# Kernel optimization log

Hardware: AMD Instinct MI355X
Metric: run time of the kernel (lower is better)

The kernel has to match this reference:

```python
import jax, jax.numpy as jnp
import numpy as np

NHEAD = 16
NUM_GROUPS = 4
EXPERTS_PER_GROUP = 2
LN_EPS = 1e-5


def _layernorm(x, g, b):
    mu = jnp.mean(x, axis=-1, keepdims=True)
    var = jnp.mean(jnp.square(x - mu), axis=-1, keepdims=True)
    return (x - mu) * jax.lax.rsqrt(var + LN_EPS) * g + b


def _mha(x, wi, bi, wo, bo):
    # torch nn.MultiheadAttention (batch_first): qkv = x @ in_proj_w.T + in_proj_b
    B, S, D = x.shape
    hd = D // NHEAD
    qkv = x @ wi.T + bi                      # [B,S,3D]
    q, k, v = jnp.split(qkv, 3, axis=-1)
    def heads(t):
        return t.reshape(B, S, NHEAD, hd).transpose(0, 2, 1, 3)  # [B,H,S,hd]
    q, k, v = heads(q), heads(k), heads(v)
    scores = jnp.einsum('bhqd,bhkd->bhqk', q, k) / jnp.sqrt(jnp.asarray(hd, x.dtype))
    attn = jax.nn.softmax(scores, axis=-1)
    o = jnp.einsum('bhqk,bhkd->bhqd', attn, v)
    o = o.transpose(0, 2, 1, 3).reshape(B, S, D)
    return o @ wo.T + bo


def _hier_moe(x, w_group, b_group, w_expert, b_expert, w1, b1, w2, b2):
    # Two-level top-1 routing: group gate -> expert gate within chosen group.
    B, S, D = x.shape
    xt = x.reshape(B * S, D)                 # [T,D]
    T = xt.shape[0]
    E = NUM_GROUPS * EXPERTS_PER_GROUP

    gp = jax.nn.softmax(xt @ w_group + b_group, axis=-1)          # [T,G]
    g_idx = jnp.argmax(gp, axis=-1)                                # [T]
    g_prob = jnp.max(gp, axis=-1)                                  # [T]

    elog = jnp.einsum('td,gde->tge', xt, w_expert) + b_expert      # [T,G,Epg]
    ep = jax.nn.softmax(elog, axis=-1)
    ep_sel = jnp.take_along_axis(ep, g_idx[:, None, None], axis=1)[:, 0, :]  # [T,Epg]
    e_idx_local = jnp.argmax(ep_sel, axis=-1)                      # [T]
    e_prob = jnp.max(ep_sel, axis=-1)                              # [T]

    flat_e = g_idx * EXPERTS_PER_GROUP + e_idx_local               # [T]
    combine = jax.nn.one_hot(flat_e, E, dtype=xt.dtype) * (g_prob * e_prob)[:, None]  # [T,E]

    # Dense dispatch (reference): run every expert on all tokens, combine with one-hot weights.
    h = jax.nn.relu(jnp.einsum('td,edf->etf', xt, w1) + b1[:, None, :])   # [E,T,Fff]
    y = jnp.einsum('etf,efd->etd', h, w2) + b2[:, None, :]                # [E,T,D]
    out = jnp.einsum('te,etd->td', combine, y)                            # [T,D]
    return out.reshape(B, S, D)


def setup_inputs() -> dict:
    key = jax.random.key(0)
    ks = jax.random.split(key, 8)
    B, S, D, F = 2, 1024, 1024, 2048
    G, Epg = NUM_GROUPS, EXPERTS_PER_GROUP
    E = G * Epg
    sc = lambda fan: 1.0 / np.sqrt(fan)
    return {
        'x': jax.random.normal(ks[0], (B, S, D), jnp.float32),
        'in_proj_w': jax.random.normal(ks[1], (3 * D, D), jnp.float32) * sc(D),
        'in_proj_b': jnp.zeros((3 * D,), jnp.float32),
        'out_proj_w': jax.random.normal(ks[2], (D, D), jnp.float32) * sc(D),
        'out_proj_b': jnp.zeros((D,), jnp.float32),
        'ln1_g': jnp.ones((D,), jnp.float32),
        'ln1_b': jnp.zeros((D,), jnp.float32),
        'ln2_g': jnp.ones((D,), jnp.float32),
        'ln2_b': jnp.zeros((D,), jnp.float32),
        'w_group': jax.random.normal(ks[3], (D, G), jnp.float32) * sc(D),
        'b_group': jnp.zeros((G,), jnp.float32),
        'w_expert': jax.random.normal(ks[4], (G, D, Epg), jnp.float32) * sc(D),
        'b_expert': jnp.zeros((G, Epg), jnp.float32),
        'w1': jax.random.normal(ks[5], (E, D, F), jnp.float32) * sc(D),
        'b1': jnp.zeros((E, F), jnp.float32),
        'w2': jax.random.normal(ks[6], (E, F, D), jnp.float32) * sc(F),
        'b2': jnp.zeros((E, D), jnp.float32),
    }


def reference(x, in_proj_w, in_proj_b, out_proj_w, out_proj_b,
              ln1_g, ln1_b, ln2_g, ln2_b,
              w_group, b_group, w_expert, b_expert, w1, b1, w2, b2):
    # Dropout p=0.1 is identity in eval mode.
    attn_out = _mha(x, in_proj_w, in_proj_b, out_proj_w, out_proj_b)
    x = _layernorm(x + attn_out, ln1_g, ln1_b)
    moe_out = _hier_moe(x, w_group, b_group, w_expert, b_expert, w1, b1, w2, b2)
    x = _layernorm(x + moe_out, ln2_g, ln2_b)
    return x
```

## Files before the change

kernel.cpp:

```cpp
#include <hip/hip_runtime.h>
#include <hip/hip_bf16.h>

#define TT 2048
#define DD 1024
#define FF 2048
#define SS 1024
#define NHD 16
#define HDD 64
#define NG 4
#define EPG 2
#define NE 8

#define QSC 0.18033688011112042f

typedef __attribute__((ext_vector_type(8))) short bf16x8;
typedef __attribute__((ext_vector_type(4))) float f32x4;
typedef __attribute__((ext_vector_type(4))) unsigned short ush4;

__device__ __forceinline__ unsigned short f2bf(float x) {
    unsigned int u = __float_as_uint(x);
    u = (u + 0x7fffu + ((u >> 16) & 1u)) >> 16;
    return (unsigned short)u;
}
__device__ __forceinline__ float bf2f(unsigned short h) {
    return __uint_as_float((unsigned int)h << 16);
}

__device__ __forceinline__ float wave_sum(float s) {
#pragma unroll
    for (int off = 32; off > 0; off >>= 1) s += __shfl_xor(s, off);
    return s;
}

__device__ __forceinline__ void gl16(const void* g, void* l) {
    auto gp = reinterpret_cast<const unsigned int __attribute__((address_space(1)))*>(
        (unsigned long long)g);
    auto lp = reinterpret_cast<unsigned int __attribute__((address_space(3)))*>(
        (unsigned int)(unsigned long long)l);
    __builtin_amdgcn_global_load_lds(gp, lp, 16, 0, 0);
}

__global__ __launch_bounds__(256) void split_bf16_kernel(
    const float* __restrict__ in, unsigned short* __restrict__ hi,
    unsigned short* __restrict__ lo, int n4)
{
    const int i = blockIdx.x * 256 + threadIdx.x;
    if (i >= n4) return;
    const float4 v = ((const float4*)in)[i];
    float vv[4] = {v.x, v.y, v.z, v.w};
    ush4 h, l;
#pragma unroll
    for (int j = 0; j < 4; ++j) {
        const unsigned short hb = f2bf(vv[j]);
        ((unsigned short*)&h)[j] = hb;
        ((unsigned short*)&l)[j] = f2bf(vv[j] - bf2f(hb));
    }
    ((ush4*)hi)[i] = h;
    ((ush4*)lo)[i] = l;
}

__global__ __launch_bounds__(256, 3) void gemm_split_kernel(
    const unsigned short* __restrict__ Ah, const unsigned short* __restrict__ Al,
    const unsigned short* __restrict__ Bh, const unsigned short* __restrict__ Bl,
    const float* __restrict__ bias, const float* __restrict__ resid,
    float* __restrict__ C, unsigned short* __restrict__ Chi,
    unsigned short* __restrict__ Clo, int qscale_n, int M, int N, int K)
{
    __shared__ unsigned short sAh[128 * 64];
    __shared__ unsigned short sAl[128 * 64];
    __shared__ unsigned short sBh[64 * 64];
    __shared__ unsigned short sBl[64 * 64];
    const int tid = threadIdx.x;
    const int lane = tid & 63, wid = tid >> 6;
    const int l15 = lane & 15, lg = lane >> 4;
    const int n0 = blockIdx.x << 6, m0 = blockIdx.y << 7;
    const int kper = K / gridDim.z;
    const int kbeg = blockIdx.z * kper, kend = kbeg + kper;
    float* __restrict__ Cz = C ? (C + (size_t)blockIdx.z * M * N) : C;

    f32x4 acc[2][4];
#pragma unroll
    for (int mi = 0; mi < 2; ++mi)
#pragma unroll
        for (int ni = 0; ni < 4; ++ni) acc[mi][ni] = (f32x4){0.f, 0.f, 0.f, 0.f};

    for (int k0 = kbeg; k0 < kend; k0 += 64) {
#pragma unroll
        for (int r = 0; r < 4; ++r) {
            const int s = (r << 8) + tid;
            const int row = s >> 3;
            const int cs = (s & 7) ^ (row & 7);
            const int lb = (s & ~63) << 3;
            const size_t ga = (size_t)(m0 + row) * K + k0 + (cs << 3);
            gl16(Ah + ga, &sAh[lb]);
            gl16(Al + ga, &sAl[lb]);
        }
#pragma unroll
        for (int r = 0; r < 2; ++r) {
            const int s = (r << 8) + tid;
            const int row = s >> 3;
            const int cs = (s & 7) ^ (row & 7);
            const int lb = (s & ~63) << 3;
            const size_t gb = (size_t)(n0 + row) * K + k0 + (cs << 3);
            gl16(Bh + gb, &sBh[lb]);
            gl16(Bl + gb, &sBl[lb]);
        }
        __syncthreads();
#pragma unroll
        for (int ks = 0; ks < 2; ++ks) {
            bf16x8 ah[2], al[2], bh[4], bl[4];
            const int ac = (ks << 2) + lg;
#pragma unroll
            for (int i = 0; i < 2; ++i) {
                const int ar = (wid << 5) + (i << 4) + l15;
                const int pa = ((ar << 3) | (ac ^ (ar & 7))) << 3;
                ah[i] = *(const bf16x8*)&sAh[pa];
                al[i] = *(const bf16x8*)&sAl[pa];
            }
#pragma unroll
            for (int i = 0; i < 4; ++i) {
                const int br = (i << 4) + l15;
                const int pb = ((br << 3) | (ac ^ (br & 7))) << 3;
                bh[i] = *(const bf16x8*)&sBh[pb];
                bl[i] = *(const bf16x8*)&sBl[pb];
            }
#pragma unroll
            for (int mi = 0; mi < 2; ++mi)
#pragma unroll
                for (int ni = 0; ni < 4; ++ni) {
                    acc[mi][ni] = __builtin_amdgcn_mfma_f32_16x16x32_bf16(ah[mi], bh[ni], acc[mi][ni], 0, 0, 0);
                    acc[mi][ni] = __builtin_amdgcn_mfma_f32_16x16x32_bf16(ah[mi], bl[ni], acc[mi][ni], 0, 0, 0);
                    acc[mi][ni] = __builtin_amdgcn_mfma_f32_16x16x32_bf16(al[mi], bh[ni], acc[mi][ni], 0, 0, 0);
                }
        }
        __syncthreads();
    }
#pragma unroll
    for (int mi = 0; mi < 2; ++mi)
#pragma unroll
        for (int ni = 0; ni < 4; ++ni)
#pragma unroll
            for (int r2 = 0; r2 < 4; ++r2) {
                const int m = m0 + (wid << 5) + (mi << 4) + (lg << 2) + r2;
                const int n = n0 + (ni << 4) + l15;
                float v = acc[mi][ni][r2];
                if (bias) v += bias[n];
                if (resid) v += resid[(size_t)m * N + n];
                const size_t idx = (size_t)m * N + n;
                if (Chi) {
                    if (n < qscale_n) v *= QSC;
                    const unsigned short hb = f2bf(v);
                    Chi[idx] = hb;
                    Clo[idx] = f2bf(v - bf2f(hb));
                } else {
                    Cz[idx] = v;
                }
            }
}

__global__ __launch_bounds__(256) void vtrans_kernel(
    const unsigned short* __restrict__ srch, const unsigned short* __restrict__ srcl,
    unsigned short* __restrict__ dsth, unsigned short* __restrict__ dstl)
{
    __shared__ unsigned short tile[64][65];
    const unsigned short* __restrict__ src = blockIdx.z ? srcl : srch;
    unsigned short* __restrict__ dst = blockIdx.z ? dstl : dsth;
    const int bh = blockIdx.y, b = bh >> 4, h = bh & 15;
    const int s0 = blockIdx.x << 6;
    const int tid = threadIdx.x;
#pragma unroll
    for (int r = 0; r < 2; ++r) {
        const int sl = tid + (r << 8);
        const int rr = sl >> 3, c8 = (sl & 7) << 3;
        const bf16x8 v = *(const bf16x8*)(src + (size_t)(b * SS + s0 + rr) * 3072 + 2048 + h * HDD + c8);
#pragma unroll
        for (int j = 0; j < 8; ++j) tile[rr][c8 + j] = ((const unsigned short*)&v)[j];
    }
    __syncthreads();
#pragma unroll
    for (int r = 0; r < 2; ++r) {
        const int sl = tid + (r << 8);
        const int d = sl >> 3, s8 = (sl & 7) << 3;
        bf16x8 o;
#pragma unroll
        for (int j = 0; j < 8; ++j) ((unsigned short*)&o)[j] = tile[s8 + j][d];
        *(bf16x8*)(dst + (size_t)(bh * HDD + d) * SS + s0 + s8) = o;
    }
}

__global__ __launch_bounds__(256, 4) void attn_mfma_kernel(
    const unsigned short* __restrict__ qh, const unsigned short* __restrict__ ql,
    const unsigned short* __restrict__ vth, const unsigned short* __restrict__ vtl,
    float* __restrict__ opart, float* __restrict__ mpart, float* __restrict__ lpart)
{
    __shared__ unsigned short sKh[4096], sKl[4096];
    __shared__ unsigned short sVh[4096], sVl[4096];
    const int bh = blockIdx.y, b = bh >> 4, h = bh & 15;
    const int q0 = blockIdx.x << 6;
    const int z = blockIdx.z;
    const int tid = threadIdx.x, lane = tid & 63, w = tid >> 6;
    const int l15 = lane & 15, lg = lane >> 4;

#pragma unroll
    for (int r = 0; r < 2; ++r) {
        const int s = (r << 8) + tid;
        const int row = s >> 3;
        const int cs = (s & 7) ^ (row & 7);
        const int lb = (s & ~63) << 3;
        const size_t gq = (size_t)(b * SS + q0 + row) * 3072 + h * HDD + (cs << 3);
        gl16(qh + gq, &sKh[lb]);
        gl16(ql + gq, &sKl[lb]);
    }
    __syncthreads();
    bf16x8 qah[2], qal[2];
#pragma unroll
    for (int ks = 0; ks < 2; ++ks) {
        const int ar = (w << 4) + l15;
        const int ac = (ks << 2) + lg;
        const int pa = ((ar << 3) | (ac ^ (ar & 7))) << 3;
        qah[ks] = *(const bf16x8*)&sKh[pa];
        qal[ks] = *(const bf16x8*)&sKl[pa];
    }
    __syncthreads();

    f32x4 accO[4];
#pragma unroll
    for (int nt = 0; nt < 4; ++nt) accO[nt] = (f32x4){0.f, 0.f, 0.f, 0.f};
    float m_run = -3.0e38f, l_run = 0.f;

    const int kvbeg = z << 9;
    for (int kv0 = kvbeg; kv0 < kvbeg + 512; kv0 += 64) {
#pragma unroll
        for (int r = 0; r < 2; ++r) {
            const int s = (r << 8) + tid;
            const int row = s >> 3;
            const int cs = (s & 7) ^ (row & 7);
            const int lb = (s & ~63) << 3;
            const size_t gk = (size_t)(b * SS + kv0 + row) * 3072 + DD + h * HDD + (cs << 3);
            gl16(qh + gk, &sKh[lb]);
            gl16(ql + gk, &sKl[lb]);
            const size_t gv = (size_t)(bh * HDD + row) * SS + kv0 + (cs << 3);
            gl16(vth + gv, &sVh[lb]);
            gl16(vtl + gv, &sVl[lb]);
        }
        __syncthreads();

        f32x4 sacc[4];
#pragma unroll
        for (int i = 0; i < 4; ++i) sacc[i] = (f32x4){0.f, 0.f, 0.f, 0.f};
        __builtin_amdgcn_s_setprio(1);
#pragma unroll
        for (int ks = 0; ks < 2; ++ks) {
            const int ac = (ks << 2) + lg;
#pragma unroll
            for (int i = 0; i < 4; ++i) {
                const int br = (i << 4) + l15;
                const int pb = ((br << 3) | (ac ^ (br & 7))) << 3;
                const bf16x8 kbh = *(const bf16x8*)&sKh[pb];
                const bf16x8 kbl = *(const bf16x8*)&sKl[pb];
                sacc[i] = __builtin_amdgcn_mfma_f32_16x16x32_bf16(kbh, qah[ks], sacc[i], 0, 0, 0);
                sacc[i] = __builtin_amdgcn_mfma_f32_16x16x32_bf16(kbh, qal[ks], sacc[i], 0, 0, 0);
                sacc[i] = __builtin_amdgcn_mfma_f32_16x16x32_bf16(kbl, qah[ks], sacc[i], 0, 0, 0);
            }
        }
        __builtin_amdgcn_s_setprio(0);
        __syncthreads();

        float mx = sacc[0][0];
#pragma unroll
        for (int i = 0; i < 4; ++i)
#pragma unroll
            for (int r2 = 0; r2 < 4; ++r2) mx = fmaxf(mx, sacc[i][r2]);
        mx = fmaxf(mx, __shfl_xor(mx, 16));
        mx = fmaxf(mx, __shfl_xor(mx, 32));
        const bool skip = __all(mx <= m_run + 8.0f);
        float mn, corr;
        if (skip) {
            mn = m_run; corr = 1.0f;
        } else {
            mn = fmaxf(m_run, mx);
            corr = exp2f(m_run - mn);
            m_run = mn;
        }
        float ls = 0.f;
        const int qrow = (w << 4) | l15;
#pragma unroll
        for (int i = 0; i < 4; ++i) {
            ush4 hp, lp;
#pragma unroll
            for (int r2 = 0; r2 < 4; ++r2) {
                const float p = exp2f(sacc[i][r2] - mn);
                ls += p;
                const unsigned short hb = (unsigned short)(__float_as_uint(p) >> 16);
                hp[r2] = hb;
                lp[r2] = (unsigned short)(__float_as_uint(p - bf2f(hb)) >> 16);
            }
            const int kvb = (i << 4) + (lg << 2);
            const int idx = (qrow << 6) + (((kvb >> 3) ^ (qrow & 7)) << 3) + (kvb & 7);
            *(ush4*)&sKh[idx] = hp;
            *(ush4*)&sKl[idx] = lp;
        }
        ls += __shfl_xor(ls, 16);
        ls += __shfl_xor(ls, 32);
        if (skip) {
            l_run += ls;
        } else {
            l_run = l_run * corr + ls;
            float c4[4];
#pragma unroll
            for (int r2 = 0; r2 < 4; ++r2)
                c4[r2] = __shfl(corr, (lane & 48) | ((lg << 2) + r2));
#pragma unroll
            for (int nt = 0; nt < 4; ++nt)
#pragma unroll
                for (int r2 = 0; r2 < 4; ++r2) accO[nt][r2] *= c4[r2];
        }

        __builtin_amdgcn_s_setprio(1);
#pragma unroll
        for (int ks = 0; ks < 2; ++ks) {
            const int qq = (w << 4) + l15;
            const int slot = (ks << 2) + lg;
            const int pidx = (qq << 6) + ((slot ^ (qq & 7)) << 3);
            const bf16x8 pah = *(const bf16x8*)&sKh[pidx];
            const bf16x8 pal = *(const bf16x8*)&sKl[pidx];
            const int ac = (ks << 2) + lg;
#pragma unroll
            for (int nt = 0; nt < 4; ++nt) {
                const int dr = (nt << 4) + l15;
                const int pv = ((dr << 3) | (ac ^ (dr & 7))) << 3;
                const bf16x8 vbh = *(const bf16x8*)&sVh[pv];
                const bf16x8 vbl = *(const bf16x8*)&sVl[pv];
                accO[nt] = __builtin_amdgcn_mfma_f32_16x16x32_bf16(pah, vbh, accO[nt], 0, 0, 0);
                accO[nt] = __builtin_amdgcn_mfma_f32_16x16x32_bf16(pah, vbl, accO[nt], 0, 0, 0);
                accO[nt] = __builtin_amdgcn_mfma_f32_16x16x32_bf16(pal, vbh, accO[nt], 0, 0, 0);
            }
        }
        __builtin_amdgcn_s_setprio(0);
        __syncthreads();
    }

#pragma unroll
    for (int nt = 0; nt < 4; ++nt)
#pragma unroll
        for (int r2 = 0; r2 < 4; ++r2) {
            const int qq = q0 + (w << 4) + (lg << 2) + r2;
            const int dd = h * HDD + (nt << 4) + l15;
            opart[((size_t)z * TT + b * SS + qq) * DD + dd] = accO[nt][r2];
        }
    if (lane < 16) {
        const int qq = q0 + (w << 4) + lane;
        const int idx = z * (32 * SS) + bh * SS + qq;
        mpart[idx] = m_run;
        lpart[idx] = l_run;
    }
}

__global__ __launch_bounds__(256) void attn_combine_kernel(
    const float* __restrict__ opart, const float* __restrict__ mpart,
    const float* __restrict__ lpart, unsigned short* __restrict__ ohi,
    unsigned short* __restrict__ olo)
{
    const int t = blockIdx.x;
    const int tid = threadIdx.x;
    const int b = t >> 10, q = t & 1023;
    const int d0 = tid << 2;
    const int bh = (b << 4) + (d0 >> 6);
    const int mi = bh * SS + q;
    const float m0 = mpart[mi], m1 = mpart[32 * SS + mi];
    const float l0 = lpart[mi], l1 = lpart[32 * SS + mi];
    const float m = fmaxf(m0, m1);
    const float e0 = exp2f(m0 - m), e1 = exp2f(m1 - m);
    const float inv = 1.0f / (l0 * e0 + l1 * e1);
    const float4 a = *(const float4*)(opart + (size_t)t * DD + d0);
    const float4 c = *(const float4*)(opart + (size_t)(TT + t) * DD + d0);
    const float vv[4] = { (a.x * e0 + c.x * e1) * inv, (a.y * e0 + c.y * e1) * inv,
                          (a.z * e0 + c.z * e1) * inv, (a.w * e0 + c.w * e1) * inv };
    ush4 hh, ll;
#pragma unroll
    for (int j = 0; j < 4; ++j) {
        const unsigned short hb = f2bf(vv[j]);
        hh[j] = hb;
        ll[j] = f2bf(vv[j] - bf2f(hb));
    }
    *(ush4*)(ohi + (size_t)t * DD + d0) = hh;
    *(ush4*)(olo + (size_t)t * DD + d0) = ll;
}

__global__ __launch_bounds__(256) void ln_kernel(
    const float* __restrict__ in, const float* __restrict__ gamma,
    const float* __restrict__ beta, float* __restrict__ outf)
{
    const int t = blockIdx.x;
    const int tid = threadIdx.x;
    __shared__ float red[8];
    const float4 v = ((const float4*)(in + (size_t)t * DD))[tid];
    float s = v.x + v.y + v.z + v.w;
    s = wave_sum(s);
    const int wid = tid >> 6, lane = tid & 63;
    if (lane == 0) red[wid] = s;
    __syncthreads();
    const float mu = (red[0] + red[1] + red[2] + red[3]) * (1.0f / DD);
    const float d0 = v.x - mu, d1 = v.y - mu, d2 = v.z - mu, d3 = v.w - mu;
    float q = d0 * d0 + d1 * d1 + d2 * d2 + d3 * d3;
    q = wave_sum(q);
    if (lane == 0) red[4 + wid] = q;
    __syncthreads();
    const float var = (red[4] + red[5] + red[6] + red[7]) * (1.0f / DD);
    const float rstd = 1.0f / sqrtf(var + 1e-5f);
    const float4 g4 = ((const float4*)gamma)[tid];
    const float4 b4 = ((const float4*)beta)[tid];
    float4 ov = { d0 * rstd * g4.x + b4.x, d1 * rstd * g4.y + b4.y,
                  d2 * rstd * g4.z + b4.z, d3 * rstd * g4.w + b4.w };
    ((float4*)(outf + (size_t)t * DD))[tid] = ov;
}

__global__ __launch_bounds__(256) void ln_route_kernel(
    const float* __restrict__ x, const float* __restrict__ p0,
    const float* __restrict__ p1, const float* __restrict__ bo,
    const float* __restrict__ gamma, const float* __restrict__ beta,
    float* __restrict__ outf, unsigned short* __restrict__ outb,
    const float* __restrict__ wg, const float* __restrict__ bg,
    const float* __restrict__ we, const float* __restrict__ be,
    int* __restrict__ eid, float* __restrict__ gate, int* __restrict__ counts)
{
    const int t = blockIdx.x;
    const int tid = threadIdx.x;
    __shared__ float red[8];
    __shared__ float red2[4][12];
    const float4 xv = ((const float4*)(x + (size_t)t * DD))[tid];
    const float4 a4 = ((const float4*)(p0 + (size_t)t * DD))[tid];
    const float4 c4v = ((const float4*)(p1 + (size_t)t * DD))[tid];
    const float4 bo4 = ((const float4*)bo)[tid];
    const float4 v = { xv.x + a4.x + c4v.x + bo4.x, xv.y + a4.y + c4v.y + bo4.y,
                       xv.z + a4.z + c4v.z + bo4.z, xv.w + a4.w + c4v.w + bo4.w };
    float s = v.x + v.y + v.z + v.w;
    s = wave_sum(s);
    const int wid = tid >> 6, lane = tid & 63;
    if (lane == 0) red[wid] = s;
    __syncthreads();
    const float mu = (red[0] + red[1] + red[2] + red[3]) * (1.0f / DD);
    const float d0 = v.x - mu, d1 = v.y - mu, d2 = v.z - mu, d3 = v.w - mu;
    float q = d0 * d0 + d1 * d1 + d2 * d2 + d3 * d3;
    q = wave_sum(q);
    if (lane == 0) red[4 + wid] = q;
    __syncthreads();
    const float var = (red[4] + red[5] + red[6] + red[7]) * (1.0f / DD);
    const float rstd = 1.0f / sqrtf(var + 1e-5f);
    const float4 g4 = ((const float4*)gamma)[tid];
    const float4 b4 = ((const float4*)beta)[tid];
    const float o0 = d0 * rstd * g4.x + b4.x;
    const float o1 = d1 * rstd * g4.y + b4.y;
    const float o2 = d2 * rstd * g4.z + b4.z;
    const float o3 = d3 * rstd * g4.w + b4.w;
    float4 ov = {o0, o1, o2, o3};
    ((float4*)(outf + (size_t)t * DD))[tid] = ov;
    ush4 wv = { f2bf(o0), f2bf(o1), f2bf(o2), f2bf(o3) };
    *(ush4*)(outb + (size_t)t * DD + (tid << 2)) = wv;

    float pz[12];
#pragma unroll
    for (int k = 0; k < 12; ++k) pz[k] = 0.f;
    const float xo[4] = {o0, o1, o2, o3};
#pragma unroll
    for (int j = 0; j < 4; ++j) {
        const int c = (tid << 2) + j;
        const float xvv = xo[j];
        const float4 wgv = *(const float4*)(wg + c * NG);
        pz[0] = fmaf(xvv, wgv.x, pz[0]);
        pz[1] = fmaf(xvv, wgv.y, pz[1]);
        pz[2] = fmaf(xvv, wgv.z, pz[2]);
        pz[3] = fmaf(xvv, wgv.w, pz[3]);
#pragma unroll
        for (int g = 0; g < NG; ++g) {
            const float2 wev = *(const float2*)(we + ((size_t)g * DD + c) * EPG);
            pz[4 + 2 * g]     = fmaf(xvv, wev.x, pz[4 + 2 * g]);
            pz[4 + 2 * g + 1] = fmaf(xvv, wev.y, pz[4 + 2 * g + 1]);
        }
    }
#pragma unroll
    for (int k = 0; k < 12; ++k) pz[k] = wave_sum(pz[k]);
    if (lane == 0) {
#pragma unroll
        for (int k = 0; k < 12; ++k) red2[wid][k] = pz[k];
    }
    __syncthreads();
    if (tid == 0) {
        float zs[12];
#pragma unroll
        for (int k = 0; k < 12; ++k)
            zs[k] = red2[0][k] + red2[1][k] + red2[2][k] + red2[3][k];
        float z[NG];
#pragma unroll
        for (int g = 0; g < NG; ++g) z[g] = zs[g] + bg[g];
        int gi = 0; float zb = z[0];
#pragma unroll
        for (int g = 1; g < NG; ++g) if (z[g] > zb) { zb = z[g]; gi = g; }
        float se = 0.f;
#pragma unroll
        for (int g = 0; g < NG; ++g) se += __expf(z[g] - zb);
        const float gprob = 1.0f / se;
        float e0 = 0.f, e1 = 0.f;
#pragma unroll
        for (int g = 0; g < NG; ++g) {
            if (g == gi) {
                e0 = zs[4 + 2 * g] + be[g * EPG + 0];
                e1 = zs[4 + 2 * g + 1] + be[g * EPG + 1];
            }
        }
        const int ei = (e1 > e0) ? 1 : 0;
        const float ehi = ei ? e1 : e0, elo = ei ? e0 : e1;
        const float eprob = 1.0f / (1.0f + __expf(elo - ehi));
        eid[t] = gi * EPG + ei;
        gate[t] = gprob * eprob;
        atomicAdd(&counts[gi * EPG + ei], 1);
    }
}

__global__ void zero_counts_kernel(int* __restrict__ counts) {
    if (threadIdx.x < NE) counts[threadIdx.x] = 0;
}

__global__ __launch_bounds__(256) void route_scatter_kernel(
    const int* __restrict__ eid, const int* __restrict__ counts,
    int* __restrict__ offs, int* __restrict__ perm)
{
    __shared__ int loff[NE + 1];
    __shared__ int lcur[NE];
    if (threadIdx.x == 0) {
        int run = 0;
        for (int e = 0; e < NE; ++e) { loff[e] = run; lcur[e] = run; run += counts[e]; }
        loff[NE] = run;
    }
    __syncthreads();
    for (int t = threadIdx.x; t < TT; t += 256) {
        const int slot = atomicAdd(&lcur[eid[t]], 1);
        perm[slot] = t;
    }
    if (threadIdx.x <= NE) offs[threadIdx.x] = loff[threadIdx.x];
}

__global__ __launch_bounds__(256) void transpose_bf16_kernel(
    const float* __restrict__ in, unsigned short* __restrict__ out, int R, int C)
{
    __shared__ unsigned short tile[64][72];
    const int c0 = blockIdx.x << 6, r0 = blockIdx.y << 6;
    const size_t bo = (size_t)blockIdx.z * R * C;
    const int tid = threadIdx.x;
#pragma unroll
    for (int p = 0; p < 4; ++p) {
        const int s = (p << 8) + tid;
        const int rr = s >> 4, cc = (s & 15) << 2;
        const float4 v = *(const float4*)(in + bo + (size_t)(r0 + rr) * C + c0 + cc);
        tile[rr][cc + 0] = f2bf(v.x);
        tile[rr][cc + 1] = f2bf(v.y);
        tile[rr][cc + 2] = f2bf(v.z);
        tile[rr][cc + 3] = f2bf(v.w);
    }
    __syncthreads();
#pragma unroll
    for (int p = 0; p < 2; ++p) {
        const int s = (p << 8) + tid;
        const int cc = s >> 3, rr = (s & 7) << 3;
        bf16x8 o;
#pragma unroll
        for (int j = 0; j < 8; ++j) ((unsigned short*)&o)[j] = tile[rr + j][cc];
        *(bf16x8*)(out + bo + (size_t)(c0 + cc) * R + r0 + rr) = o;
    }
}

__global__ __launch_bounds__(256, 3) void moe_gemm1_kernel(
    const unsigned short* __restrict__ x1b, const unsigned short* __restrict__ w1t,
    const float* __restrict__ b1, const int* __restrict__ offs,
    const int* __restrict__ perm, unsigned short* __restrict__ hbuf)
{
    const int e = blockIdx.y >> 4, mt = blockIdx.y & 15;
    const int row0 = offs[e] + (mt << 7);
    const int rend = offs[e + 1];
    if (row0 >= rend) return;
    const int valid = min(rend - row0, 128);
    const int n0 = blockIdx.x << 6;
    __shared__ unsigned short sA[2][128 * 64];
    __shared__ unsigned short sB[2][64 * 64];
    const int tid = threadIdx.x;
    const int lane = tid & 63, wid = tid >> 6;
    const int l15 = lane & 15, lg = lane >> 4;
    const int wr = wid >> 1, wc = wid & 1;

    size_t abase[4];
    int albs[4];
#pragma unroll
    for (int r = 0; r < 4; ++r) {
        const int s = (r << 8) + tid;
        const int row = s >> 3;
        const int cs = (s & 7) ^ (row & 7);
        albs[r] = (s & ~63) << 3;
        const int tk = perm[min(row0 + row, rend - 1)];
        abase[r] = (size_t)tk * DD + (cs << 3);
    }
    size_t bbase[2];
    int blbs[2];
#pragma unroll
    for (int r = 0; r < 2; ++r) {
        const int s = (r << 8) + tid;
        const int row = s >> 3;
        const int cs = (s & 7) ^ (row & 7);
        blbs[r] = (s & ~63) << 3;
        bbase[r] = ((size_t)e * FF + n0 + row) * DD + (cs << 3);
    }

    f32x4 acc[4][2];
#pragma unroll
    for (int mi = 0; mi < 4; ++mi)
#pragma unroll
        for (int ni = 0; ni < 2; ++ni) acc[mi][ni] = (f32x4){0.f, 0.f, 0.f, 0.f};

#pragma unroll
    for (int r = 0; r < 4; ++r) gl16(x1b + abase[r], &sA[0][albs[r]]);
#pragma unroll
    for (int r = 0; r < 2; ++r) gl16(w1t + bbase[r], &sB[0][blbs[r]]);
    __syncthreads();
    int cur = 0;
    for (int k0 = 0; k0 < DD; k0 += 64) {
        const int nxt = k0 + 64;
        if (nxt < DD) {
#pragma unroll
            for (int r = 0; r < 4; ++r) gl16(x1b + abase[r] + nxt, &sA[cur ^ 1][albs[r]]);
#pragma unroll
            for (int r = 0; r < 2; ++r) gl16(w1t + bbase[r] + nxt, &sB[cur ^ 1][blbs[r]]);
        }
#pragma unroll
        for (int ks = 0; ks < 2; ++ks) {
            const int ac = (ks << 2) + lg;
            bf16x8 a[4], bb[2];
#pragma unroll
            for (int mi = 0; mi < 4; ++mi) {
                const int ar = (wr << 6) + (mi << 4) + l15;
                const int pa = ((ar << 3) | (ac ^ (ar & 7))) << 3;
                a[mi] = *(const bf16x8*)&sA[cur][pa];
            }
#pragma unroll
            for (int ni = 0; ni < 2; ++ni) {
                const int br = (wc << 5) + (ni << 4) + l15;
                const int pb = ((br << 3) | (ac ^ (br & 7))) << 3;
                bb[ni] = *(const bf16x8*)&sB[cur][pb];
            }
#pragma unroll
            for (int mi = 0; mi < 4; ++mi)
#pragma unroll
                for (int ni = 0; ni < 2; ++ni)
                    acc[mi][ni] = __builtin_amdgcn_mfma_f32_16x16x32_bf16(a[mi], bb[ni], acc[mi][ni], 0, 0, 0);
        }
        __syncthreads();
        cur ^= 1;
    }

    const float* bias = b1 + e * FF + n0;
#pragma unroll
    for (int mi = 0; mi < 4; ++mi)
#pragma unroll
        for (int ni = 0; ni < 2; ++ni) {
            const int n = (wc << 5) + (ni << 4) + l15;
#pragma unroll
            for (int r2 = 0; r2 < 4; ++r2) {
                const int m = (wr << 6) + (mi << 4) + (lg << 2) + r2;
                if (m < valid) {
                    float v = fmaxf(acc[mi][ni][r2] + bias[n], 0.f);
                    hbuf[(size_t)(row0 + m) * FF + n0 + n] = f2bf(v);
                }
            }
        }
}

__global__ __launch_bounds__(256, 3) void moe_gemm2_kernel(
    const unsigned short* __restrict__ hbuf, const unsigned short* __restrict__ w2t,
    const int* __restrict__ offs, float* __restrict__ p0, float* __restrict__ p1)
{
    const int e = blockIdx.y >> 4, mt = blockIdx.y & 15;
    const int row0 = offs[e] + (mt << 7);
    const int rend = offs[e + 1];
    if (row0 >= rend) return;
    const int valid = min(rend - row0, 128);
    const int n0 = blockIdx.x << 6;
    const int z = blockIdx.z;
    float* __restrict__ pbuf = z ? p1 : p0;
    __shared__ unsigned short sA[2][128 * 64];
    __shared__ unsigned short sB[2][64 * 64];
    const int tid = threadIdx.x;
    const int lane = tid & 63, wid = tid >> 6;
    const int l15 = lane & 15, lg = lane >> 4;
    const int wr = wid >> 1, wc = wid & 1;

    size_t abase[4];
    int albs[4];
#pragma unroll
    for (int r = 0; r < 4; ++r) {
        const int s = (r << 8) + tid;
        const int row = s >> 3;
        const int cs = (s & 7) ^ (row & 7);
        albs[r] = (s & ~63) << 3;
        abase[r] = (size_t)min(row0 + row, rend - 1) * FF + (cs << 3);
    }
    size_t bbase[2];
    int blbs[2];
#pragma unroll
    for (int r = 0; r < 2; ++r) {
        const int s = (r << 8) + tid;
        const int row = s >> 3;
        const int cs = (s & 7) ^ (row & 7);
        blbs[r] = (s & ~63) << 3;
        bbase[r] = ((size_t)e * DD + n0 + row) * FF + (cs << 3);
    }

    f32x4 acc[4][2];
#pragma unroll
    for (int mi = 0; mi < 4; ++mi)
#pragma unroll
        for (int ni = 0; ni < 2; ++ni) acc[mi][ni] = (f32x4){0.f, 0.f, 0.f, 0.f};

    const int kbeg = z << 10, kend = kbeg + 1024;
#pragma unroll
    for (int r = 0; r < 4; ++r) gl16(hbuf + abase[r] + kbeg, &sA[0][albs[r]]);
#pragma unroll
    for (int r = 0; r < 2; ++r) gl16(w2t + bbase[r] + kbeg, &sB[0][blbs[r]]);
    __syncthreads();
    int cur = 0;
    for (int k0 = kbeg; k0 < kend; k0 += 64) {
        const int nxt = k0 + 64;
        if (nxt < kend) {
#pragma unroll
            for (int r = 0; r < 4; ++r) gl16(hbuf + abase[r] + nxt, &sA[cur ^ 1][albs[r]]);
#pragma unroll
            for (int r = 0; r < 2; ++r) gl16(w2t + bbase[r] + nxt, &sB[cur ^ 1][blbs[r]]);
        }
#pragma unroll
        for (int ks = 0; ks < 2; ++ks) {
            const int ac = (ks << 2) + lg;
            bf16x8 a[4], bb[2];
#pragma unroll
            for (int mi = 0; mi < 4; ++mi) {
                const int ar = (wr << 6) + (mi << 4) + l15;
                const int pa = ((ar << 3) | (ac ^ (ar & 7))) << 3;
                a[mi] = *(const bf16x8*)&sA[cur][pa];
            }
#pragma unroll
            for (int ni = 0; ni < 2; ++ni) {
                const int br = (wc << 5) + (ni << 4) + l15;
                const int pb = ((br << 3) | (ac ^ (br & 7))) << 3;
                bb[ni] = *(const bf16x8*)&sB[cur][pb];
            }
#pragma unroll
            for (int mi = 0; mi < 4; ++mi)
#pragma unroll
                for (int ni = 0; ni < 2; ++ni)
                    acc[mi][ni] = __builtin_amdgcn_mfma_f32_16x16x32_bf16(a[mi], bb[ni], acc[mi][ni], 0, 0, 0);
        }
        __syncthreads();
        cur ^= 1;
    }

#pragma unroll
    for (int mi = 0; mi < 4; ++mi)
#pragma unroll
        for (int ni = 0; ni < 2; ++ni) {
            const int n = (wc << 5) + (ni << 4) + l15;
#pragma unroll
            for (int r2 = 0; r2 < 4; ++r2) {
                const int m = (wr << 6) + (mi << 4) + (lg << 2) + r2;
                if (m < valid) pbuf[(size_t)(row0 + m) * DD + n0 + n] = acc[mi][ni][r2];
            }
        }
}

__global__ __launch_bounds__(256) void moe2_combine_kernel(
    const float* __restrict__ p0, const float* __restrict__ p1,
    const int* __restrict__ offs, const int* __restrict__ perm,
    const float* __restrict__ gate, const float* __restrict__ b2,
    const float* __restrict__ x1, float* __restrict__ res2)
{
    const int s = blockIdx.x;
    const int tid = threadIdx.x;
    int e = 0;
#pragma unroll
    for (int g = 1; g < NE; ++g) e += (s >= offs[g]) ? 1 : 0;
    const int tk = perm[s];
    const float gt = gate[tk];
    const int c0 = tid << 2;
    const float4 a  = *(const float4*)(p0 + (size_t)s * DD + c0);
    const float4 b  = *(const float4*)(p1 + (size_t)s * DD + c0);
    const float4 bb = *(const float4*)(b2 + (size_t)e * DD + c0);
    const float4 xx = *(const float4*)(x1 + (size_t)tk * DD + c0);
    float4 o = { xx.x + gt * (a.x + b.x + bb.x), xx.y + gt * (a.y + b.y + bb.y),
                 xx.z + gt * (a.z + b.z + bb.z), xx.w + gt * (a.w + b.w + bb.w) };
    *(float4*)(res2 + (size_t)tk * DD + c0) = o;
}

extern "C" void kernel_launch(void* const* d_in, const int* in_sizes, int n_in,
                              void* d_out, int out_size, void* d_ws, size_t ws_size,
                              hipStream_t stream)
{
    (void)in_sizes; (void)n_in; (void)out_size; (void)ws_size;
    const float* x   = (const float*)d_in[0];
    const float* wi  = (const float*)d_in[1];
    const float* bi  = (const float*)d_in[2];
    const float* wo  = (const float*)d_in[3];
    const float* bo  = (const float*)d_in[4];
    const float* g1  = (const float*)d_in[5];
    const float* be1 = (const float*)d_in[6];
    const float* g2  = (const float*)d_in[7];
    const float* be2 = (const float*)d_in[8];
    const float* wgr = (const float*)d_in[9];
    const float* bgr = (const float*)d_in[10];
    const float* wex = (const float*)d_in[11];
    const float* bex = (const float*)d_in[12];
    const float* w1  = (const float*)d_in[13];
    const float* b1  = (const float*)d_in[14];
    const float* w2  = (const float*)d_in[15];
    const float* b2  = (const float*)d_in[16];
    float* out = (float*)d_out;

    char* ws = (char*)d_ws;
    unsigned short* qkvh  = (unsigned short*)(ws + 0);
    unsigned short* qkvl  = (unsigned short*)(ws + 12582912);
    unsigned short* hbuf  = (unsigned short*)(ws + 0);
    float* res2           = (float*)(ws + 8388608);
    unsigned short* vth   = (unsigned short*)(ws + 25165824);
    unsigned short* vtl   = (unsigned short*)(ws + 29360128);
    float* x1             = (float*)(ws + 41943040);
    unsigned short* x1b   = (unsigned short*)(ws + 50331648);
    unsigned short* w1t   = (unsigned short*)(ws + 54525952);
    unsigned short* w2t   = (unsigned short*)(ws + 88080384);
    char* misc = ws + 121634816;
    int*   eid    = (int*)(misc);
    float* gate   = (float*)(misc + 8192);
    int*   perm   = (int*)(misc + 16384);
    int*   counts = (int*)(misc + 24576);
    int*   offs   = (int*)(misc + 24640);

    unsigned short* xs_hi = (unsigned short*)(ws + 33554432);
    unsigned short* xs_lo = (unsigned short*)(ws + 33554432 + 4194304);
    unsigned short* wi_hi = (unsigned short*)(ws + 54525952);
    unsigned short* wi_lo = (unsigned short*)(ws + 54525952 + 6291456);
    unsigned short* o_hi  = (unsigned short*)(ws + 41943040);
    unsigned short* o_lo  = (unsigned short*)(ws + 41943040 + 4194304);
    unsigned short* wo_hi = (unsigned short*)(ws + 88080384);
    unsigned short* wo_lo = (unsigned short*)(ws + 88080384 + 2097152);

    float* opart = (float*)(ws + 54525952);
    float* mpart = (float*)(ws + 54525952 + 16777216);
    float* lpart = (float*)(ws + 54525952 + 17039360);

    float* oproj = (float*)(ws + 0);

    float* mp0 = (float*)(ws + 16777216);
    float* mp1 = (float*)(ws + 25165824);

    zero_counts_kernel<<<dim3(1), dim3(64), 0, stream>>>(counts);

    split_bf16_kernel<<<dim3((TT * DD / 4 + 255) / 256), dim3(256), 0, stream>>>(x, xs_hi, xs_lo, TT * DD / 4);
    split_bf16_kernel<<<dim3((3 * DD * DD / 4 + 255) / 256), dim3(256), 0, stream>>>(wi, wi_hi, wi_lo, 3 * DD * DD / 4);
    gemm_split_kernel<<<dim3(3 * DD / 64, TT / 128, 1), dim3(256), 0, stream>>>(
        xs_hi, xs_lo, wi_hi, wi_lo, bi, (const float*)nullptr,
        (float*)nullptr, qkvh, qkvl, DD, TT, 3 * DD, DD);

    vtrans_kernel<<<dim3(SS / 64, 2 * NHD, 2), dim3(256), 0, stream>>>(qkvh, qkvl, vth, vtl);

    attn_mfma_kernel<<<dim3(SS / 64, 2 * NHD, 2), dim3(256), 0, stream>>>(
        qkvh, qkvl, vth, vtl, opart, mpart, lpart);
    attn_combine_kernel<<<dim3(TT), dim3(256), 0, stream>>>(opart, mpart, lpart, o_hi, o_lo);

    split_bf16_kernel<<<dim3((DD * DD / 4 + 255) / 256), dim3(256), 0, stream>>>(wo, wo_hi, wo_lo, DD * DD / 4);
    gemm_split_kernel<<<dim3(DD / 64, TT / 128, 2), dim3(256), 0, stream>>>(
        o_hi, o_lo, wo_hi, wo_lo, (const float*)nullptr, (const float*)nullptr,
        oproj, (unsigned short*)nullptr, (unsigned short*)nullptr, 0, TT, DD, DD);

    ln_route_kernel<<<dim3(TT), dim3(256), 0, stream>>>(
        x, oproj, oproj + (size_t)TT * DD, bo, g1, be1, x1, x1b,
        wgr, bgr, wex, bex, eid, gate, counts);
    route_scatter_kernel<<<dim3(1), dim3(256), 0, stream>>>(eid, counts, offs, perm);

    transpose_bf16_kernel<<<dim3(FF / 64, DD / 64, NE), dim3(256), 0, stream>>>(w1, w1t, DD, FF);
    transpose_bf16_kernel<<<dim3(DD / 64, FF / 64, NE), dim3(256), 0, stream>>>(w2, w2t, FF, DD);

    moe_gemm1_kernel<<<dim3(FF / 64, NE * 16), dim3(256), 0, stream>>>(x1b, w1t, b1, offs, perm, hbuf);
    moe_gemm2_kernel<<<dim3(DD / 64, NE * 16, 2), dim3(256), 0, stream>>>(hbuf, w2t, offs, mp0, mp1);
    moe2_combine_kernel<<<dim3(TT), dim3(256), 0, stream>>>(mp0, mp1, offs, perm, gate, b2, x1, res2);

    ln_kernel<<<dim3(TT), dim3(256), 0, stream>>>(res2, g2, be2, out);
}
```

Before: 253.0 us.

## Double attention query tile per block and merge small prep kernels

The attention kernel now processes 128 query rows per block, two 16-row groups per wave, so each K/V tile loaded into LDS is reused twice. P gets its own LDS buffers and occupancy drops to 2 blocks per CU. Separately, the three bf16 split launches plus the counts-zeroing kernel are merged into one launch, and the two weight transposes into one. This cuts launch overhead and K/V reload traffic at the cost of more registers and LDS per block and half as many attention blocks.

Result: faster. 241.6 us (-4.5%).

```diff
diff --git a/kernel.cpp b/kernel.cpp
--- a/kernel.cpp
+++ b/kernel.cpp
@@ -40,23 +40,36 @@
     __builtin_amdgcn_global_load_lds(gp, lp, 16, 0, 0);
 }
 
-__global__ __launch_bounds__(256) void split_bf16_kernel(
-    const float* __restrict__ in, unsigned short* __restrict__ hi,
-    unsigned short* __restrict__ lo, int n4)
-{
+#define NX4 (TT * DD / 4)
+#define NWI4 (3 * DD * DD / 4)
+#define NWO4 (DD * DD / 4)
+__global__ __launch_bounds__(256) void split3_kernel(
+    const float* __restrict__ x, const float* __restrict__ wi,
+    const float* __restrict__ wo,
+    unsigned short* __restrict__ xs_hi, unsigned short* __restrict__ xs_lo,
+    unsigned short* __restrict__ wi_hi, unsigned short* __restrict__ wi_lo,
+    unsigned short* __restrict__ wo_hi, unsigned short* __restrict__ wo_lo,
+    int* __restrict__ counts)
+{
+    if (blockIdx.x == 0 && threadIdx.x < NE) counts[threadIdx.x] = 0;
     const int i = blockIdx.x * 256 + threadIdx.x;
-    if (i >= n4) return;
-    const float4 v = ((const float4*)in)[i];
+    const float* in;
+    unsigned short *hi, *lo;
+    int j;
+    if (i < NX4) { in = x; hi = xs_hi; lo = xs_lo; j = i; }
+    else if (i < NX4 + NWI4) { in = wi; hi = wi_hi; lo = wi_lo; j = i - NX4; }
+    else { in = wo; hi = wo_hi; lo = wo_lo; j = i - NX4 - NWI4; }
+    const float4 v = ((const float4*)in)[j];
     float vv[4] = {v.x, v.y, v.z, v.w};
     ush4 h, l;
 #pragma unroll
-    for (int j = 0; j < 4; ++j) {
-        const unsigned short hb = f2bf(vv[j]);
-        ((unsigned short*)&h)[j] = hb;
-        ((unsigned short*)&l)[j] = f2bf(vv[j] - bf2f(hb));
-    }
-    ((ush4*)hi)[i] = h;
-    ((ush4*)lo)[i] = l;
+    for (int k = 0; k < 4; ++k) {
+        const unsigned short hb = f2bf(vv[k]);
+        ((unsigned short*)&h)[k] = hb;
+        ((unsigned short*)&l)[k] = f2bf(vv[k] - bf2f(hb));
+    }
+    ((ush4*)hi)[j] = h;
+    ((ush4*)lo)[j] = l;
 }
 
 __global__ __launch_bounds__(256, 3) void gemm_split_kernel(
@@ -188,45 +201,49 @@
     }
 }
 
-__global__ __launch_bounds__(256, 4) void attn_mfma_kernel(
+__global__ __launch_bounds__(256, 2) void attn_mfma_kernel(
     const unsigned short* __restrict__ qh, const unsigned short* __restrict__ ql,
     const unsigned short* __restrict__ vth, const unsigned short* __restrict__ vtl,
     float* __restrict__ opart, float* __restrict__ mpart, float* __restrict__ lpart)
 {
     __shared__ unsigned short sKh[4096], sKl[4096];
     __shared__ unsigned short sVh[4096], sVl[4096];
+    __shared__ unsigned short sPh[8192], sPl[8192];
     const int bh = blockIdx.y, b = bh >> 4, h = bh & 15;
-    const int q0 = blockIdx.x << 6;
+    const int q0 = blockIdx.x << 7;
     const int z = blockIdx.z;
     const int tid = threadIdx.x, lane = tid & 63, w = tid >> 6;
     const int l15 = lane & 15, lg = lane >> 4;
 
 #pragma unroll
-    for (int r = 0; r < 2; ++r) {
+    for (int r = 0; r < 4; ++r) {
         const int s = (r << 8) + tid;
         const int row = s >> 3;
         const int cs = (s & 7) ^ (row & 7);
         const int lb = (s & ~63) << 3;
         const size_t gq = (size_t)(b * SS + q0 + row) * 3072 + h * HDD + (cs << 3);
-        gl16(qh + gq, &sKh[lb]);
-        gl16(ql + gq, &sKl[lb]);
-    }
-    __syncthreads();
-    bf16x8 qah[2], qal[2];
-#pragma unroll
-    for (int ks = 0; ks < 2; ++ks) {
-        const int ar = (w << 4) + l15;
-        const int ac = (ks << 2) + lg;
-        const int pa = ((ar << 3) | (ac ^ (ar & 7))) << 3;
-        qah[ks] = *(const bf16x8*)&sKh[pa];
-        qal[ks] = *(const bf16x8*)&sKl[pa];
-    }
-    __syncthreads();
-
-    f32x4 accO[4];
-#pragma unroll
-    for (int nt = 0; nt < 4; ++nt) accO[nt] = (f32x4){0.f, 0.f, 0.f, 0.f};
-    float m_run = -3.0e38f, l_run = 0.f;
+        gl16(qh + gq, &sPh[lb]);
+        gl16(ql + gq, &sPl[lb]);
+    }
+    __syncthreads();
+    bf16x8 qah[2][2], qal[2][2];
+#pragma unroll
+    for (int g = 0; g < 2; ++g)
+#pragma unroll
+        for (int ks = 0; ks < 2; ++ks) {
+            const int ar = (w << 5) + (g << 4) + l15;
+            const int ac = (ks << 2) + lg;
+            const int pa = ((ar << 3) | (ac ^ (ar & 7))) << 3;
+            qah[g][ks] = *(const bf16x8*)&sPh[pa];
+            qal[g][ks] = *(const bf16x8*)&sPl[pa];
+        }
+
+    f32x4 accO[2][4];
+#pragma unroll
+    for (int g = 0; g < 2; ++g)
+#pragma unroll
+        for (int nt = 0; nt < 4; ++nt) accO[g][nt] = (f32x4){0.f, 0.f, 0.f, 0.f};
+    float m_run[2] = {-3.0e38f, -3.0e38f}, l_run[2] = {0.f, 0.f};
 
     const int kvbeg = z << 9;
     for (int kv0 = kvbeg; kv0 < kvbeg + 512; kv0 += 64) {
@@ -245,9 +262,11 @@
         }
         __syncthreads();
 
-        f32x4 sacc[4];
-#pragma unroll
-        for (int i = 0; i < 4; ++i) sacc[i] = (f32x4){0.f, 0.f, 0.f, 0.f};
+        f32x4 sacc[2][4];
+#pragma unroll
+        for (int g = 0; g < 2; ++g)
+#pragma unroll
+            for (int i = 0; i < 4; ++i) sacc[g][i] = (f32x4){0.f, 0.f, 0.f, 0.f};
         __builtin_amdgcn_s_setprio(1);
 #pragma unroll
         for (int ks = 0; ks < 2; ++ks) {
@@ -258,72 +277,82 @@
                 const int pb = ((br << 3) | (ac ^ (br & 7))) << 3;
                 const bf16x8 kbh = *(const bf16x8*)&sKh[pb];
                 const bf16x8 kbl = *(const bf16x8*)&sKl[pb];
-                sacc[i] = __builtin_amdgcn_mfma_f32_16x16x32_bf16(kbh, qah[ks], sacc[i], 0, 0, 0);
-                sacc[i] = __builtin_amdgcn_mfma_f32_16x16x32_bf16(kbh, qal[ks], sacc[i], 0, 0, 0);
-                sacc[i] = __builtin_amdgcn_mfma_f32_16x16x32_bf16(kbl, qah[ks], sacc[i], 0, 0, 0);
+#pragma unroll
+                for (int g = 0; g < 2; ++g) {
+                    sacc[g][i] = __builtin_amdgcn_mfma_f32_16x16x32_bf16(kbh, qah[g][ks], sacc[g][i], 0, 0, 0);
+                    sacc[g][i] = __builtin_amdgcn_mfma_f32_16x16x32_bf16(kbh, qal[g][ks], sacc[g][i], 0, 0, 0);
+                    sacc[g][i] = __builtin_amdgcn_mfma_f32_16x16x32_bf16(kbl, qah[g][ks], sacc[g][i], 0, 0, 0);
+                }
             }
         }
         __builtin_amdgcn_s_setprio(0);
         __syncthreads();
 
-        float mx = sacc[0][0];
-#pragma unroll
-        for (int i = 0; i < 4; ++i)
-#pragma unroll
-            for (int r2 = 0; r2 < 4; ++r2) mx = fmaxf(mx, sacc[i][r2]);
-        mx = fmaxf(mx, __shfl_xor(mx, 16));
-        mx = fmaxf(mx, __shfl_xor(mx, 32));
-        const bool skip = __all(mx <= m_run + 8.0f);
-        float mn, corr;
-        if (skip) {
-            mn = m_run; corr = 1.0f;
-        } else {
-            mn = fmaxf(m_run, mx);
-            corr = exp2f(m_run - mn);
-            m_run = mn;
-        }
-        float ls = 0.f;
-        const int qrow = (w << 4) | l15;
-#pragma unroll
-        for (int i = 0; i < 4; ++i) {
-            ush4 hp, lp;
-#pragma unroll
-            for (int r2 = 0; r2 < 4; ++r2) {
-                const float p = exp2f(sacc[i][r2] - mn);
-                ls += p;
-                const unsigned short hb = (unsigned short)(__float_as_uint(p) >> 16);
-                hp[r2] = hb;
-                lp[r2] = (unsigned short)(__float_as_uint(p - bf2f(hb)) >> 16);
-            }
-            const int kvb = (i << 4) + (lg << 2);
-            const int idx = (qrow << 6) + (((kvb >> 3) ^ (qrow & 7)) << 3) + (kvb & 7);
-            *(ush4*)&sKh[idx] = hp;
-            *(ush4*)&sKl[idx] = lp;
-        }
-        ls += __shfl_xor(ls, 16);
-        ls += __shfl_xor(ls, 32);
-        if (skip) {
-            l_run += ls;
-        } else {
-            l_run = l_run * corr + ls;
-            float c4[4];
-#pragma unroll
-            for (int r2 = 0; r2 < 4; ++r2)
-                c4[r2] = __shfl(corr, (lane & 48) | ((lg << 2) + r2));
-#pragma unroll
-            for (int nt = 0; nt < 4; ++nt)
-#pragma unroll
-                for (int r2 = 0; r2 < 4; ++r2) accO[nt][r2] *= c4[r2];
+#pragma unroll
+        for (int g = 0; g < 2; ++g) {
+            float mx = sacc[g][0][0];
+#pragma unroll
+            for (int i = 0; i < 4; ++i)
+#pragma unroll
+                for (int r2 = 0; r2 < 4; ++r2) mx = fmaxf(mx, sacc[g][i][r2]);
+            mx = fmaxf(mx, __shfl_xor(mx, 16));
+            mx = fmaxf(mx, __shfl_xor(mx, 32));
+            const bool skip = __all(mx <= m_run[g] + 8.0f);
+            float mn, corr;
+            if (skip) {
+                mn = m_run[g]; corr = 1.0f;
+            } else {
+                mn = fmaxf(m_run[g], mx);
+                corr = exp2f(m_run[g] - mn);
+                m_run[g] = mn;
+            }
+            float ls = 0.f;
+            const int qrow = (w << 5) + (g << 4) + l15;
+#pragma unroll
+            for (int i = 0; i < 4; ++i) {
+                ush4 hp, lp;
+#pragma unroll
+                for (int r2 = 0; r2 < 4; ++r2) {
+                    const float p = exp2f(sacc[g][i][r2] - mn);
+                    ls += p;
+                    const unsigned short hb = (unsigned short)(__float_as_uint(p) >> 16);
+                    hp[r2] = hb;
+                    lp[r2] = (unsigned short)(__float_as_uint(p - bf2f(hb)) >> 16);
+                }
+                const int kvb = (i << 4) + (lg << 2);
+                const int idx = (qrow << 6) + (((kvb >> 3) ^ (qrow & 7)) << 3) + (kvb & 7);
+                *(ush4*)&sPh[idx] = hp;
+                *(ush4*)&sPl[idx] = lp;
+            }
+            ls += __shfl_xor(ls, 16);
+            ls += __shfl_xor(ls, 32);
+            if (skip) {
+                l_run[g] += ls;
+            } else {
+                l_run[g] = l_run[g] * corr + ls;
+                float c4[4];
+#pragma unroll
+                for (int r2 = 0; r2 < 4; ++r2)
+                    c4[r2] = __shfl(corr, (lane & 48) | ((lg << 2) + r2));
+#pragma unroll
+                for (int nt = 0; nt < 4; ++nt)
+#pragma unroll
+                    for (int r2 = 0; r2 < 4; ++r2) accO[g][nt][r2] *= c4[r2];
+            }
         }
 
         __builtin_amdgcn_s_setprio(1);
 #pragma unroll
         for (int ks = 0; ks < 2; ++ks) {
-            const int qq = (w << 4) + l15;
-            const int slot = (ks << 2) + lg;
-            const int pidx = (qq << 6) + ((slot ^ (qq & 7)) << 3);
-            const bf16x8 pah = *(const bf16x8*)&sKh[pidx];
-            const bf16x8 pal = *(const bf16x8*)&sKl[pidx];
+            bf16x8 pah[2], pal[2];
+#pragma unroll
+            for (int g = 0; g < 2; ++g) {
+                const int qq = (w << 5) + (g << 4) + l15;
+                const int slot = (ks << 2) + lg;
+                const int pidx = (qq << 6) + ((slot ^ (qq & 7)) << 3);
+                pah[g] = *(const bf16x8*)&sPh[pidx];
+                pal[g] = *(const bf16x8*)&sPl[pidx];
+            }
             const int ac = (ks << 2) + lg;
 #pragma unroll
             for (int nt = 0; nt < 4; ++nt) {
@@ -331,9 +360,12 @@
                 const int pv = ((dr << 3) | (ac ^ (dr & 7))) << 3;
                 const bf16x8 vbh = *(const bf16x8*)&sVh[pv];
                 const bf16x8 vbl = *(const bf16x8*)&sVl[pv];
-                accO[nt] = __builtin_amdgcn_mfma_f32_16x16x32_bf16(pah, vbh, accO[nt], 0, 0, 0);
-                accO[nt] = __builtin_amdgcn_mfma_f32_16x16x32_bf16(pah, vbl, accO[nt], 0, 0, 0);
-                accO[nt] = __builtin_amdgcn_mfma_f32_16x16x32_bf16(pal, vbh, accO[nt], 0, 0, 0);
+#pragma unroll
+                for (int g = 0; g < 2; ++g) {
+                    accO[g][nt] = __builtin_amdgcn_mfma_f32_16x16x32_bf16(pah[g], vbh, accO[g][nt], 0, 0, 0);
+                    accO[g][nt] = __builtin_amdgcn_mfma_f32_16x16x32_bf16(pah[g], vbl, accO[g][nt], 0, 0, 0);
+                    accO[g][nt] = __builtin_amdgcn_mfma_f32_16x16x32_bf16(pal[g], vbh, accO[g][nt], 0, 0, 0);
+                }
             }
         }
         __builtin_amdgcn_s_setprio(0);
@@ -341,18 +373,23 @@
     }
 
 #pragma unroll
-    for (int nt = 0; nt < 4; ++nt)
-#pragma unroll
-        for (int r2 = 0; r2 < 4; ++r2) {
-            const int qq = q0 + (w << 4) + (lg << 2) + r2;
-            const int dd = h * HDD + (nt << 4) + l15;
-            opart[((size_t)z * TT + b * SS + qq) * DD + dd] = accO[nt][r2];
-        }
+    for (int g = 0; g < 2; ++g)
+#pragma unroll
+        for (int nt = 0; nt < 4; ++nt)
+#pragma unroll
+            for (int r2 = 0; r2 < 4; ++r2) {
+                const int qq = q0 + (w << 5) + (g << 4) + (lg << 2) + r2;
+                const int dd = h * HDD + (nt << 4) + l15;
+                opart[((size_t)z * TT + b * SS + qq) * DD + dd] = accO[g][nt][r2];
+            }
     if (lane < 16) {
-        const int qq = q0 + (w << 4) + lane;
-        const int idx = z * (32 * SS) + bh * SS + qq;
-        mpart[idx] = m_run;
-        lpart[idx] = l_run;
+#pragma unroll
+        for (int g = 0; g < 2; ++g) {
+            const int qq = q0 + (w << 5) + (g << 4) + lane;
+            const int idx = z * (32 * SS) + bh * SS + qq;
+            mpart[idx] = m_run[g];
+            lpart[idx] = l_run[g];
+        }
     }
 }
 
@@ -517,10 +554,6 @@
     }
 }
 
-__global__ void zero_counts_kernel(int* __restrict__ counts) {
-    if (threadIdx.x < NE) counts[threadIdx.x] = 0;
-}
-
 __global__ __launch_bounds__(256) void route_scatter_kernel(
     const int* __restrict__ eid, const int* __restrict__ counts,
     int* __restrict__ offs, int* __restrict__ perm)
@@ -540,18 +573,27 @@
     if (threadIdx.x <= NE) offs[threadIdx.x] = loff[threadIdx.x];
 }
 
-__global__ __launch_bounds__(256) void transpose_bf16_kernel(
-    const float* __restrict__ in, unsigned short* __restrict__ out, int R, int C)
+__global__ __launch_bounds__(256) void transpose_both_kernel(
+    const float* __restrict__ w1, const float* __restrict__ w2,
+    unsigned short* __restrict__ w1t, unsigned short* __restrict__ w2t)
 {
     __shared__ unsigned short tile[64][72];
-    const int c0 = blockIdx.x << 6, r0 = blockIdx.y << 6;
-    const size_t bo = (size_t)blockIdx.z * R * C;
+    const int yz = blockIdx.y;
+    const bool is1 = yz < NE;
+    const int e = is1 ? yz : yz - NE;
+    const int R = is1 ? DD : FF;
+    const int C = is1 ? FF : DD;
+    const float* __restrict__ in = (is1 ? w1 : w2) + (size_t)e * DD * FF;
+    unsigned short* __restrict__ out = (is1 ? w1t : w2t) + (size_t)e * DD * FF;
+    const int nbx = C >> 6;
+    const int c0 = (blockIdx.x % nbx) << 6;
+    const int r0 = (blockIdx.x / nbx) << 6;
     const int tid = threadIdx.x;
 #pragma unroll
     for (int p = 0; p < 4; ++p) {
         const int s = (p << 8) + tid;
         const int rr = s >> 4, cc = (s & 15) << 2;
-        const float4 v = *(const float4*)(in + bo + (size_t)(r0 + rr) * C + c0 + cc);
+        const float4 v = *(const float4*)(in + (size_t)(r0 + rr) * C + c0 + cc);
         tile[rr][cc + 0] = f2bf(v.x);
         tile[rr][cc + 1] = f2bf(v.y);
         tile[rr][cc + 2] = f2bf(v.z);
@@ -565,7 +607,7 @@
         bf16x8 o;
 #pragma unroll
         for (int j = 0; j < 8; ++j) ((unsigned short*)&o)[j] = tile[rr + j][cc];
-        *(bf16x8*)(out + bo + (size_t)(c0 + cc) * R + r0 + rr) = o;
+        *(bf16x8*)(out + (size_t)(c0 + cc) * R + r0 + rr) = o;
     }
 }
 
@@ -855,21 +897,19 @@
     float* mp0 = (float*)(ws + 16777216);
     float* mp1 = (float*)(ws + 25165824);
 
-    zero_counts_kernel<<<dim3(1), dim3(64), 0, stream>>>(counts);
-
-    split_bf16_kernel<<<dim3((TT * DD / 4 + 255) / 256), dim3(256), 0, stream>>>(x, xs_hi, xs_lo, TT * DD / 4);
-    split_bf16_kernel<<<dim3((3 * DD * DD / 4 + 255) / 256), dim3(256), 0, stream>>>(wi, wi_hi, wi_lo, 3 * DD * DD / 4);
+    split3_kernel<<<dim3((NX4 + NWI4 + NWO4) / 256), dim3(256), 0, stream>>>(
+        x, wi, wo, xs_hi, xs_lo, wi_hi, wi_lo, wo_hi, wo_lo, counts);
+
     gemm_split_kernel<<<dim3(3 * DD / 64, TT / 128, 1), dim3(256), 0, stream>>>(
         xs_hi, xs_lo, wi_hi, wi_lo, bi, (const float*)nullptr,
         (float*)nullptr, qkvh, qkvl, DD, TT, 3 * DD, DD);
 
     vtrans_kernel<<<dim3(SS / 64, 2 * NHD, 2), dim3(256), 0, stream>>>(qkvh, qkvl, vth, vtl);
 
-    attn_mfma_kernel<<<dim3(SS / 64, 2 * NHD, 2), dim3(256), 0, stream>>>(
+    attn_mfma_kernel<<<dim3(SS / 128, 2 * NHD, 2), dim3(256), 0, stream>>>(
         qkvh, qkvl, vth, vtl, opart, mpart, lpart);
     attn_combine_kernel<<<dim3(TT), dim3(256), 0, stream>>>(opart, mpart, lpart, o_hi, o_lo);
 
-    split_bf16_kernel<<<dim3((DD * DD / 4 + 255) / 256), dim3(256), 0, stream>>>(wo, wo_hi, wo_lo, DD * DD / 4);
     gemm_split_kernel<<<dim3(DD / 64, TT / 128, 2), dim3(256), 0, stream>>>(
         o_hi, o_lo, wo_hi, wo_lo, (const float*)nullptr, (const float*)nullptr,
         oproj, (unsigned short*)nullptr, (unsigned short*)nullptr, 0, TT, DD, DD);
@@ -879,8 +919,7 @@
         wgr, bgr, wex, bex, eid, gate, counts);
     route_scatter_kernel<<<dim3(1), dim3(256), 0, stream>>>(eid, counts, offs, perm);
 
-    transpose_bf16_kernel<<<dim3(FF / 64, DD / 64, NE), dim3(256), 0, stream>>>(w1, w1t, DD, FF);
-    transpose_bf16_kernel<<<dim3(DD / 64, FF / 64, NE), dim3(256), 0, stream>>>(w2, w2t, FF, DD);
+    transpose_both_kernel<<<dim3(512, 2 * NE), dim3(256), 0, stream>>>(w1, w2, w1t, w2t);
 
     moe_gemm1_kernel<<<dim3(FF / 64, NE * 16), dim3(256), 0, stream>>>(x1b, w1t, b1, offs, perm, hbuf);
     moe_gemm2_kernel<<<dim3(DD / 64, NE * 16, 2), dim3(256), 0, stream>>>(hbuf, w2t, offs, mp0, mp1);
```
